# Performance work log

Measured on AMD Instinct MI355X. Metric: run time of the kernel, lower is better.

## Reference

```python
import jax, jax.numpy as jnp
import numpy as np

NUM_HIDDENS = 512
NUM_HEADS = 8
B, LQ, LK = 2, 128, 128
NEG_INF = -1e6  # d2l masked_softmax fill value


def setup_inputs() -> dict:
    key = jax.random.key(0)
    ks = jax.random.split(key, 12)
    D = NUM_HIDDENS
    dh = D // NUM_HEADS
    s = 1.0 / np.sqrt(D)
    sh = 1.0 / np.sqrt(dh)
    return {
        "queries": jax.random.normal(ks[0], (B, LQ, D), jnp.float32),
        "keys": jax.random.normal(ks[1], (B, LK, D), jnp.float32),
        "values": jax.random.normal(ks[2], (B, LK, D), jnp.float32),
        "valid_lens": jax.random.randint(ks[3], (B,), 1, LK + 1, jnp.int32),
        # outer QKV/O projections (num_hiddens -> num_hiddens, no bias)
        "Wq": jax.random.normal(ks[4], (D, D), jnp.float32) * s,
        "Wk": jax.random.normal(ks[5], (D, D), jnp.float32) * s,
        "Wv": jax.random.normal(ks[6], (D, D), jnp.float32) * s,
        "Wo": jax.random.normal(ks[7], (D, D), jnp.float32) * s,
        # Bahdanau (additive) attention params: per-head dim dh -> D features
        "Wqa": jax.random.normal(ks[8], (D, dh), jnp.float32) * sh,
        "Wka": jax.random.normal(ks[9], (D, dh), jnp.float32) * sh,
        "wv_a": jax.random.normal(ks[10], (D,), jnp.float32) * s,
    }


def _split_heads(x):
    # (B, L, D) -> (B, H, L, dh)
    b, l, d = x.shape
    return x.reshape(b, l, NUM_HEADS, d // NUM_HEADS).transpose(0, 2, 1, 3)


def reference(queries, keys, values, valid_lens, Wq, Wk, Wv, Wo, Wqa, Wka, wv_a):
    # QKV projections + head split
    q = _split_heads(queries @ Wq.T)  # (B,H,Lq,dh)
    k = _split_heads(keys @ Wk.T)     # (B,H,Lk,dh)
    v = _split_heads(values @ Wv.T)   # (B,H,Lk,dh)

    # Bahdanau additive scores: wv . tanh(Wqa q + Wka k)
    qf = jnp.einsum('bhqd,fd->bhqf', q, Wqa)  # (B,H,Lq,F)
    kf = jnp.einsum('bhkd,fd->bhkf', k, Wka)  # (B,H,Lk,F)
    feat = jnp.tanh(qf[:, :, :, None, :] + kf[:, :, None, :, :])  # (B,H,Lq,Lk,F)
    scores = jnp.einsum('bhqkf,f->bhqk', feat, wv_a)  # (B,H,Lq,Lk)

    # masked softmax over keys: positions >= valid_len[b] get -1e6
    mask = jnp.arange(scores.shape[-1])[None, None, None, :] < valid_lens[:, None, None, None]
    scores = jnp.where(mask, scores, NEG_INF)
    attn = jax.nn.softmax(scores, axis=-1)

    out = jnp.einsum('bhqk,bhkd->bhqd', attn, v)  # (B,H,Lq,dh)
    b, h, lq, dh = out.shape
    out = out.transpose(0, 2, 1, 3).reshape(b, lq, h * dh)  # concat heads
    return out @ Wo.T
```

## Files before the change

kernel.cpp:

```cpp
#include <hip/hip_runtime.h>


#define NHEADS 8
#define DH 64
#define DM 512
#define BB 2
#define LQL 128
#define LKL 128
#define QPB 4

typedef _Float16 v8h __attribute__((ext_vector_type(8)));
typedef _Float16 v4h __attribute__((ext_vector_type(4)));
typedef float v4f __attribute__((ext_vector_type(4)));

static __device__ __forceinline__ float fexp2(float x) { return __builtin_amdgcn_exp2f(x); }
static __device__ __forceinline__ float frcp(float x)  { return __builtin_amdgcn_rcpf(x); }

static __device__ __forceinline__ v8h cvt8(const float4 a, const float4 b) {
    v8h h;
    h[0] = (_Float16)a.x; h[1] = (_Float16)a.y; h[2] = (_Float16)a.z; h[3] = (_Float16)a.w;
    h[4] = (_Float16)b.x; h[5] = (_Float16)b.y; h[6] = (_Float16)b.z; h[7] = (_Float16)b.w;
    return h;
}
static __device__ __forceinline__ v4h cvt4(const float4 a) {
    v4h h;
    h[0] = (_Float16)a.x; h[1] = (_Float16)a.y;
    h[2] = (_Float16)a.z; h[3] = (_Float16)a.w;
    return h;
}

static __device__ __forceinline__ unsigned short f2bf(float x) {
    unsigned int u = __float_as_uint(x);
    u += 0x7FFFu + ((u >> 16) & 1u);
    return (unsigned short)(u >> 16);
}
static __device__ __forceinline__ float bflo(unsigned int u) {
    return __uint_as_float(u << 16);
}
static __device__ __forceinline__ float bfhi(unsigned int u) {
    return __uint_as_float(u & 0xFFFF0000u);
}

__global__ __launch_bounds__(256) void qkvfeat_mfma(
    const float* __restrict__ xq, const float* __restrict__ xk, const float* __restrict__ xv,
    const float* __restrict__ Wq, const float* __restrict__ Wk, const float* __restrict__ Wv,
    const float* __restrict__ Wqa, const float* __restrict__ Wka,
    const int* __restrict__ vl,
    float* __restrict__ V, float* __restrict__ eqf, unsigned short* __restrict__ ekf)
{
    const float C2 = 2.8853900818f;
    const int bid = blockIdx.x;
    const int mat = bid >> 5;
    const int sub = bid & 31;
    const int b  = sub >> 4;
    const int hc = (sub >> 1) & 7;
    const int lh = sub & 1;
    if (mat >= 1 && lh * 64 >= vl[b]) return;

    const float* X = mat == 0 ? xq : (mat == 1 ? xk : xv);
    const float* W = mat == 0 ? Wq : (mat == 1 ? Wk : Wv);

    __shared__ _Float16 As[64][72];
    __shared__ _Float16 Ws[64][72];
    __shared__ _Float16 Qt[64][72];
    __shared__ _Float16 W2[64][72];

    const int tid = threadIdx.x, wave = tid >> 6, lane = tid & 63;
    const int srow = tid >> 2, sseg16 = (tid & 3) * 16;
    const int fr = lane & 15, fg = (lane >> 4) * 8;
    const int xrow0 = b * LQL + lh * 64;
    const int wrow0 = hc * 64;

    v4f acc[4] = {};
    for (int k0 = 0; k0 < DM; k0 += 64) {
        const float4* ap = (const float4*)(X + (size_t)(xrow0 + srow) * DM + k0 + sseg16);
        const float4 a0 = ap[0], a1 = ap[1], a2 = ap[2], a3 = ap[3];
        const float4* wp = (const float4*)(W + (size_t)(wrow0 + srow) * DM + k0 + sseg16);
        const float4 w0 = wp[0], w1 = wp[1], w2 = wp[2], w3 = wp[3];
        __syncthreads();
        *(v8h*)&As[srow][sseg16]     = cvt8(a0, a1);
        *(v8h*)&As[srow][sseg16 + 8] = cvt8(a2, a3);
        *(v8h*)&Ws[srow][sseg16]     = cvt8(w0, w1);
        *(v8h*)&Ws[srow][sseg16 + 8] = cvt8(w2, w3);
        __syncthreads();
        #pragma unroll
        for (int kk = 0; kk < 2; ++kk) {
            const v8h af = *(const v8h*)&As[wave * 16 + fr][kk * 32 + fg];
            #pragma unroll
            for (int sn = 0; sn < 4; ++sn) {
                const v8h bf = *(const v8h*)&Ws[sn * 16 + fr][kk * 32 + fg];
                acc[sn] = __builtin_amdgcn_mfma_f32_16x16x32_f16(af, bf, acc[sn], 0, 0, 0);
            }
        }
    }

    if (mat == 2) {
        #pragma unroll
        for (int sn = 0; sn < 4; ++sn)
            #pragma unroll
            for (int rg = 0; rg < 4; ++rg) {
                const int row = xrow0 + wave * 16 + (lane >> 4) * 4 + rg;
                const int col = hc * 64 + sn * 16 + fr;
                V[(size_t)row * DM + col] = acc[sn][rg];
            }
        return;
    }

    #pragma unroll
    for (int sn = 0; sn < 4; ++sn)
        #pragma unroll
        for (int rg = 0; rg < 4; ++rg)
            Qt[wave * 16 + (lane >> 4) * 4 + rg][sn * 16 + fr] = (_Float16)acc[sn][rg];

    const float* Wa = mat == 0 ? Wqa : Wka;
    const int crow0 = (b * NHEADS + hc) * LQL + lh * 64;
    const int r2 = tid >> 2, cs = (tid & 3) * 16;
    for (int ft = 0; ft < 8; ++ft) {
        const float4* wp = (const float4*)(Wa + (size_t)(ft * 64 + r2) * DH + cs);
        const float4 w0 = wp[0], w1 = wp[1], w2 = wp[2], w3 = wp[3];
        __syncthreads();
        *(v8h*)&W2[r2][cs]     = cvt8(w0, w1);
        *(v8h*)&W2[r2][cs + 8] = cvt8(w2, w3);
        __syncthreads();
        v4f fa[4] = {};
        #pragma unroll
        for (int kk = 0; kk < 2; ++kk) {
            const v8h af = *(const v8h*)&Qt[wave * 16 + fr][kk * 32 + fg];
            #pragma unroll
            for (int sn = 0; sn < 4; ++sn) {
                const v8h bf = *(const v8h*)&W2[sn * 16 + fr][kk * 32 + fg];
                fa[sn] = __builtin_amdgcn_mfma_f32_16x16x32_f16(af, bf, fa[sn], 0, 0, 0);
            }
        }
        #pragma unroll
        for (int sn = 0; sn < 4; ++sn)
            #pragma unroll
            for (int rg = 0; rg < 4; ++rg) {
                const int row = crow0 + wave * 16 + (lane >> 4) * 4 + rg;
                const int col = ft * 64 + sn * 16 + fr;
                const float ev = fexp2(C2 * fa[sn][rg]);
                if (mat == 0) eqf[(size_t)row * DM + col] = ev;
                else          ekf[(size_t)row * DM + col] = f2bf(ev);
            }
    }
}

__global__ __launch_bounds__(512, 2) void attn_kernel(
    const float* __restrict__ eqf, const unsigned short* __restrict__ ekf,
    const float* __restrict__ V, const float* __restrict__ wv_a,
    const int* __restrict__ vl, _Float16* __restrict__ interh)
{
    __shared__ float s_eq[QPB][DM];
    __shared__ float s_wv2[DM];
    __shared__ float s_part[4][QPB][132];
    __shared__ float s_attn[QPB][LKL];
    __shared__ float s_pv[2][QPB][DH];

    const float LOG2E = 1.4426950409f;

    const int bid = blockIdx.x;
    const int b  = bid >> 8;
    const int h  = (bid >> 5) & 7;
    const int qt = bid & 31;
    const int qbase = qt * QPB;
    const int bh = b * NHEADS + h;
    const int t = threadIdx.x;
    const int Lv = vl[b];

    {
        const int r = t >> 7, cc = (t & 127) * 4;
        *(float4*)&s_eq[r][cc] =
            *(const float4*)(eqf + ((size_t)(bh * LQL + qbase + r)) * DM + cc);
        s_wv2[t] = wv_a[t] * -2.0f;
    }
    __syncthreads();

    const int w = t >> 6, lane = t & 63;
    const int k  = w * 16 + (lane & 15);
    const int fq = lane >> 4;
    float acc[QPB] = {};
    if (k < Lv) {
        const unsigned short* kp = ekf + ((size_t)(bh * LKL + k)) * DM + fq * 128;
        uint4 kc = *(const uint4*)kp;
        #pragma unroll 1
        for (int it = 0; it < 16; ++it) {
            uint4 nx;
            if (it < 15) nx = *(const uint4*)(kp + 8);
            else         nx = kc;
            const float e0 = bflo(kc.x), e1 = bfhi(kc.x);
            const float e2 = bflo(kc.y), e3 = bfhi(kc.y);
            const float e4 = bflo(kc.z), e5 = bfhi(kc.z);
            const float e6 = bflo(kc.w), e7 = bfhi(kc.w);
            const int f0 = fq * 128 + it * 8;
            const float4 w0 = *(const float4*)&s_wv2[f0];
            const float4 w1 = *(const float4*)&s_wv2[f0 + 4];
            #pragma unroll
            for (int q = 0; q < QPB; ++q) {
                const float4 q0 = *(const float4*)&s_eq[q][f0];
                const float4 q1 = *(const float4*)&s_eq[q][f0 + 4];
                float a = acc[q];
                a = fmaf(w0.x, frcp(fmaf(e0, q0.x, 1.f)), a);
                a = fmaf(w0.y, frcp(fmaf(e1, q0.y, 1.f)), a);
                a = fmaf(w0.z, frcp(fmaf(e2, q0.z, 1.f)), a);
                a = fmaf(w0.w, frcp(fmaf(e3, q0.w, 1.f)), a);
                a = fmaf(w1.x, frcp(fmaf(e4, q1.x, 1.f)), a);
                a = fmaf(w1.y, frcp(fmaf(e5, q1.y, 1.f)), a);
                a = fmaf(w1.z, frcp(fmaf(e6, q1.z, 1.f)), a);
                a = fmaf(w1.w, frcp(fmaf(e7, q1.w, 1.f)), a);
                acc[q] = a;
            }
            kc = nx; kp += 8;
        }
    }
    #pragma unroll
    for (int q = 0; q < QPB; ++q) s_part[fq][q][k] = acc[q];
    __syncthreads();

    if (t < 64 * QPB) {
        const int q = t >> 6, ln = t & 63;
        float v0 = -3.0e38f, v1 = -3.0e38f;
        if (ln < Lv)
            v0 = s_part[0][q][ln] + s_part[1][q][ln]
               + s_part[2][q][ln] + s_part[3][q][ln];
        if (ln + 64 < Lv)
            v1 = s_part[0][q][ln+64] + s_part[1][q][ln+64]
               + s_part[2][q][ln+64] + s_part[3][q][ln+64];
        float m = fmaxf(v0, v1);
        #pragma unroll
        for (int off = 32; off; off >>= 1) m = fmaxf(m, __shfl_xor(m, off, 64));
        const float e0 = fexp2((v0 - m) * LOG2E);
        const float e1 = fexp2((v1 - m) * LOG2E);
        float s = e0 + e1;
        #pragma unroll
        for (int off = 32; off; off >>= 1) s += __shfl_xor(s, off, 64);
        const float inv = frcp(s);
        s_attn[q][ln]      = e0 * inv;
        s_attn[q][ln + 64] = e1 * inv;
    }
    __syncthreads();

    {
        const int d = t & 63, q = (t >> 6) & 3, kh = t >> 8;
        const float* vb = V + ((size_t)(b * LKL + kh * 64)) * DM + h * DH + d;
        int kmax = Lv - kh * 64;
        kmax = kmax < 0 ? 0 : (kmax > 64 ? 64 : kmax);
        float a0 = 0.f, a1 = 0.f, a2 = 0.f, a3 = 0.f;
        int kk = 0;
        for (; kk + 4 <= kmax; kk += 4) {
            a0 += s_attn[q][kh*64 + kk+0] * vb[(size_t)(kk+0) * DM];
            a1 += s_attn[q][kh*64 + kk+1] * vb[(size_t)(kk+1) * DM];
            a2 += s_attn[q][kh*64 + kk+2] * vb[(size_t)(kk+2) * DM];
            a3 += s_attn[q][kh*64 + kk+3] * vb[(size_t)(kk+3) * DM];
        }
        for (; kk < kmax; ++kk) a0 += s_attn[q][kh*64 + kk] * vb[(size_t)kk * DM];
        s_pv[kh][q][d] = (a0 + a1) + (a2 + a3);
    }
    __syncthreads();
    if (t < 64 * QPB) {
        const int q = t >> 6, d = t & 63;
        interh[((size_t)(b * LQL + qbase + q)) * DM + h * DH + d] =
            (_Float16)(s_pv[0][q][d] + s_pv[1][q][d]);
    }
}

__global__ __launch_bounds__(256) void out_mfma(
    const _Float16* __restrict__ interh, const float* __restrict__ Wo,
    float* __restrict__ out)
{
    const int bm0 = blockIdx.y * 32, bn0 = blockIdx.x * 32;
    __shared__ _Float16 As[32][40];
    __shared__ _Float16 Ws[32][40];
    const int tid = threadIdx.x, wave = tid >> 6, lane = tid & 63;
    const int ms = wave & 1, ns = wave >> 1;
    const int srow = tid >> 3, sseg = tid & 7;
    const int fr = lane & 15, fg = (lane >> 4) * 8;

    v4f acc = {};
    for (int k0 = 0; k0 < DM; k0 += 32) {
        const v4h ha = *(const v4h*)(interh + (size_t)(bm0 + srow) * DM + k0 + sseg * 4);
        const float4 w4 = *(const float4*)(Wo + (size_t)(bn0 + srow) * DM + k0 + sseg * 4);
        __syncthreads();
        *(v4h*)&As[srow][sseg * 4] = ha;
        *(v4h*)&Ws[srow][sseg * 4] = cvt4(w4);
        __syncthreads();
        const v8h af = *(const v8h*)&As[ms * 16 + fr][fg];
        const v8h bf = *(const v8h*)&Ws[ns * 16 + fr][fg];
        acc = __builtin_amdgcn_mfma_f32_16x16x32_f16(af, bf, acc, 0, 0, 0);
    }
    #pragma unroll
    for (int rg = 0; rg < 4; ++rg) {
        const int row = bm0 + ms * 16 + (lane >> 4) * 4 + rg;
        const int col = bn0 + ns * 16 + fr;
        out[(size_t)row * DM + col] = acc[rg];
    }
}

extern "C" void kernel_launch(void* const* d_in, const int* in_sizes, int n_in,
                              void* d_out, int out_size, void* d_ws, size_t ws_size,
                              hipStream_t stream)
{
    const float* xq   = (const float*)d_in[0];
    const float* xk   = (const float*)d_in[1];
    const float* xv   = (const float*)d_in[2];
    const int*   vl   = (const int*)d_in[3];
    const float* Wq   = (const float*)d_in[4];
    const float* Wk   = (const float*)d_in[5];
    const float* Wv   = (const float*)d_in[6];
    const float* Wo   = (const float*)d_in[7];
    const float* Wqa  = (const float*)d_in[8];
    const float* Wka  = (const float*)d_in[9];
    const float* wv_a = (const float*)d_in[10];
    float* out = (float*)d_out;

    char* base = (char*)d_ws;
    float*          V      = (float*)         (base);
    float*          eqf    = (float*)         (base + 524288);
    unsigned short* ekf    = (unsigned short*)(base + 4718592);
    _Float16*       interh = (_Float16*)      (base + 6815744);

    qkvfeat_mfma<<<dim3(96), dim3(256), 0, stream>>>(
        xq, xk, xv, Wq, Wk, Wv, Wqa, Wka, vl, V, eqf, ekf);
    attn_kernel<<<dim3(512), dim3(512), 0, stream>>>(
        eqf, ekf, V, wv_a, vl, interh);
    out_mfma<<<dim3(16, 8), dim3(256), 0, stream>>>(interh, Wo, out);
}
```

Before: 52.83 us.

## Split Q/K feature blocks by feature half, shuffle-reduce partial scores, swizzle attn grid

The projection kernel now gives the Q and K matrices twice as many blocks, each computing half of the Bahdanau feature tiles. The grid grows from 96 to 160 blocks, at the cost of recomputing the 64x64 projection tile in both halves. In the attention kernel, the per-wave partial score sums are combined with cross-lane shuffles instead of a 4-way shared-memory partial buffer. Block indices are also remapped so consecutive launched blocks are spread across batch, head and query tiles, aiming for better load balance across compute units.

```diff
diff --git a/kernel.cpp b/kernel.cpp
--- a/kernel.cpp
+++ b/kernel.cpp
@@ -50,11 +50,22 @@
 {
     const float C2 = 2.8853900818f;
     const int bid = blockIdx.x;
-    const int mat = bid >> 5;
-    const int sub = bid & 31;
-    const int b  = sub >> 4;
-    const int hc = (sub >> 1) & 7;
-    const int lh = sub & 1;
+    int mat, b, hc, lh, fh;
+    if (bid < 128) {
+        mat = bid >> 6;
+        const int sub = bid & 63;
+        b  = sub >> 5;
+        hc = (sub >> 2) & 7;
+        lh = (sub >> 1) & 1;
+        fh = sub & 1;
+    } else {
+        mat = 2;
+        const int sub = bid - 128;
+        b  = sub >> 4;
+        hc = (sub >> 1) & 7;
+        lh = sub & 1;
+        fh = 0;
+    }
     if (mat >= 1 && lh * 64 >= vl[b]) return;
 
     const float* X = mat == 0 ? xq : (mat == 1 ? xk : xv);
@@ -115,7 +126,7 @@
     const float* Wa = mat == 0 ? Wqa : Wka;
     const int crow0 = (b * NHEADS + hc) * LQL + lh * 64;
     const int r2 = tid >> 2, cs = (tid & 3) * 16;
-    for (int ft = 0; ft < 8; ++ft) {
+    for (int ft = fh * 4; ft < fh * 4 + 4; ++ft) {
         const float4* wp = (const float4*)(Wa + (size_t)(ft * 64 + r2) * DH + cs);
         const float4 w0 = wp[0], w1 = wp[1], w2 = wp[2], w3 = wp[3];
         __syncthreads();
@@ -152,13 +163,13 @@
 {
     __shared__ float s_eq[QPB][DM];
     __shared__ float s_wv2[DM];
-    __shared__ float s_part[4][QPB][132];
+    __shared__ float s_score[QPB][132];
     __shared__ float s_attn[QPB][LKL];
     __shared__ float s_pv[2][QPB][DH];
 
     const float LOG2E = 1.4426950409f;
 
-    const int bid = blockIdx.x;
+    const int bid = (blockIdx.x & 7) * 64 + (blockIdx.x >> 3);
     const int b  = bid >> 8;
     const int h  = (bid >> 5) & 7;
     const int qt = bid & 31;
@@ -213,18 +224,18 @@
         }
     }
     #pragma unroll
-    for (int q = 0; q < QPB; ++q) s_part[fq][q][k] = acc[q];
+    for (int q = 0; q < QPB; ++q) {
+        float a = acc[q];
+        a += __shfl_xor(a, 16, 64);
+        a += __shfl_xor(a, 32, 64);
+        if (lane < 16) s_score[q][k] = a;
+    }
     __syncthreads();
 
     if (t < 64 * QPB) {
         const int q = t >> 6, ln = t & 63;
-        float v0 = -3.0e38f, v1 = -3.0e38f;
-        if (ln < Lv)
-            v0 = s_part[0][q][ln] + s_part[1][q][ln]
-               + s_part[2][q][ln] + s_part[3][q][ln];
-        if (ln + 64 < Lv)
-            v1 = s_part[0][q][ln+64] + s_part[1][q][ln+64]
-               + s_part[2][q][ln+64] + s_part[3][q][ln+64];
+        const float v0 = (ln < Lv)      ? s_score[q][ln]      : -3.0e38f;
+        const float v1 = (ln + 64 < Lv) ? s_score[q][ln + 64] : -3.0e38f;
         float m = fmaxf(v0, v1);
         #pragma unroll
         for (int off = 32; off; off >>= 1) m = fmaxf(m, __shfl_xor(m, off, 64));
@@ -318,7 +329,7 @@
     unsigned short* ekf    = (unsigned short*)(base + 4718592);
     _Float16*       interh = (_Float16*)      (base + 6815744);
 
-    qkvfeat_mfma<<<dim3(96), dim3(256), 0, stream>>>(
+    qkvfeat_mfma<<<dim3(160), dim3(256), 0, stream>>>(
         xq, xk, xv, Wq, Wk, Wv, Wqa, Wka, vl, V, eqf, ekf);
     attn_kernel<<<dim3(512), dim3(512), 0, stream>>>(
         eqf, ekf, V, wv_a, vl, interh);
```

After: 44.77 us. -15.2%, faster.
